# Optimization experiments

Measured on AMD Instinct MI355X. Metric: run time of the kernel, lower is better.

The kernel has to match this reference:

```python
import jax, jax.numpy as jnp
import numpy as np

N_NODES, N_EDGES, B = 50000, 400000, 64
E, NF, G, H, MLP_H, OUT, NUM_MP = 64, 128, 128, 128, 256, 1, 2


def _lin(key, fin, fout):
    W = jax.random.normal(key, (fin, fout), dtype=jnp.float32) * jnp.sqrt(2.0 / (fin + fout))
    b = jnp.full((fout,), 0.01, dtype=jnp.float32)
    return W, b


def setup_inputs() -> dict:
    key = jax.random.key(0)
    ks = jax.random.split(key, 16)
    inp = {
        "x": jax.random.normal(ks[0], (N_NODES, NF), dtype=jnp.float32),
        "edge_index": jax.random.randint(ks[1], (2, N_EDGES), 0, N_NODES, dtype=jnp.int32),
        "edge_attr": jax.random.normal(ks[2], (N_EDGES, E), dtype=jnp.float32),
        "batch": jnp.sort(jax.random.randint(ks[3], (N_NODES,), 0, B, dtype=jnp.int32)),
    }
    # EdgeModel: Lin(E+2*NF, H), Lin(H, E)
    inp["eW0"], inp["eb0"] = _lin(ks[4], E + 2 * NF, H)
    inp["eW1"], inp["eb1"] = _lin(ks[5], H, E)
    # NodeModel mlp1: Lin(E+NF, H), Lin(H, H); mlp2: Lin(H+NF, H), Lin(H, NF)
    inp["n1W0"], inp["n1b0"] = _lin(ks[6], E + NF, H)
    inp["n1W1"], inp["n1b1"] = _lin(ks[7], H, H)
    inp["n2W0"], inp["n2b0"] = _lin(ks[8], H + NF, H)
    inp["n2W1"], inp["n2b1"] = _lin(ks[9], H, NF)
    # GlobalModel mlp1: Lin(E+NF, H), Lin(H, H); mlp2: Lin(H+NF, H), Lin(H, G)
    inp["g1W0"], inp["g1b0"] = _lin(ks[10], E + NF, H)
    inp["g1W1"], inp["g1b1"] = _lin(ks[11], H, H)
    inp["g2W0"], inp["g2b0"] = _lin(ks[12], H + NF, H)
    inp["g2W1"], inp["g2b1"] = _lin(ks[13], H, G)
    # last_mlp: Lin(G, MLP_H), Lin(MLP_H, OUT)
    inp["fW0"], inp["fb0"] = _lin(ks[14], G, MLP_H)
    inp["fW1"], inp["fb1"] = _lin(ks[15], MLP_H, OUT)
    return inp


def _forward(x, edge_attr, row, col, batch,
             eW0, eb0, eW1, eb1, n1W0, n1b0, n1W1, n1b1, n2W0, n2b0, n2W1, n2b1,
             g1W0, g1b0, g1W1, g1b1, g2W0, g2b0, g2W1, g2b1, fW0, fb0, fW1, fb1):
    ea = edge_attr
    for _ in range(NUM_MP):
        # EdgeModel: gather endpoints, concat, 2-layer MLP (no activation per config)
        ea = jnp.concatenate([x[row], x[col], ea], axis=1) @ eW0 + eb0
        ea = ea @ eW1 + eb1  # [N_EDGES, E]
        # NodeModel: per-edge msg -> scatter-add to dest (col) -> node update
        m = jnp.concatenate([x[row], ea], axis=1) @ n1W0 + n1b0
        m = m @ n1W1 + n1b1
        agg = jax.ops.segment_sum(m, col, num_segments=N_NODES)  # [N_NODES, H]
        x = jnp.concatenate([x, agg], axis=1) @ n2W0 + n2b0
        x = x @ n2W1 + n2b1  # [N_NODES, NF]
        # GlobalModel: edge msg -> scatter to nodes -> pool nodes & msgs per graph
        g = jnp.concatenate([x[row], ea], axis=1) @ g1W0 + g1b0
        g = g @ g1W1 + g1b1
        gagg = jax.ops.segment_sum(g, col, num_segments=N_NODES)
        node_pool = jax.ops.segment_sum(x, batch, num_segments=B)    # [B, NF]
        msg_pool = jax.ops.segment_sum(gagg, batch, num_segments=B)  # [B, H]
        u = jnp.concatenate([node_pool, msg_pool], axis=1) @ g2W0 + g2b0
        u = u @ g2W1 + g2b1  # [B, G]
    out = (u @ fW0 + fb0) @ fW1 + fb1  # [B, OUT]
    return out


def reference(x, edge_index, edge_attr, batch,
              eW0, eb0, eW1, eb1, n1W0, n1b0, n1W1, n1b1, n2W0, n2b0, n2W1, n2b1,
              g1W0, g1b0, g1W1, g1b1, g2W0, g2b0, g2W1, g2b1, fW0, fb0, fW1, fb1):
    row, col = edge_index[0], edge_index[1]
    return _forward(x, edge_attr, row, col, batch,
                    eW0, eb0, eW1, eb1, n1W0, n1b0, n1W1, n1b1, n2W0, n2b0, n2W1, n2b1,
                    g1W0, g1b0, g1W1, g1b1, g2W0, g2b0, g2W1, g2b1, fW0, fb0, fW1, fb1)
```

## Files before the change

### kernel.cpp

```cpp
#include <hip/hip_runtime.h>
#include <hip/hip_bf16.h>

#define N_NODES 50000
#define N_EDGES 400000
#define NB 64
#define SCB 196
#define CGB 512

typedef unsigned short u16;
typedef unsigned int u32;
typedef __attribute__((ext_vector_type(8))) short s16x8;
typedef __attribute__((ext_vector_type(4))) float f32x4;

__device__ __forceinline__ u16 f2b(float f) {
  __hip_bfloat16 h = __float2bfloat16(f);
  return *reinterpret_cast<const u16*>(&h);
}
__device__ __forceinline__ float b2f(u16 u) {
  u32 v = ((u32)u) << 16;
  return *reinterpret_cast<const float*>(&v);
}
__device__ __forceinline__ s16x8 scl8(s16x8 v, float dg) {
  s16x8 r;
#pragma unroll
  for (int i = 0; i < 8; ++i) {
    float f = b2f((u16)v[i]) * dg;
    r[i] = (short)f2b(f);
  }
  return r;
}

__global__ void k_f2b(const float* __restrict__ in, u16* __restrict__ out, int n) {
  int i = blockIdx.x * 256 + threadIdx.x;
  if (i < n) out[i] = f2b(in[i]);
}

struct MMOp { const float* A; const float* B; const float* add; float* C;
              int lda, r0, ldb, K2, N, rows; };
struct MMBatch { MMOp op[13]; };

__global__ void k_mmb(MMBatch mb) {
  MMOp o = mb.op[blockIdx.y];
  int i = blockIdx.x;
  int n = threadIdx.x;
  if (i >= o.rows || n >= o.N) return;
  float acc = o.add ? o.add[(size_t)i * o.N + n] : 0.f;
  for (int k = 0; k < o.K2; ++k)
    acc = fmaf(o.A[(size_t)(o.r0 + i) * o.lda + k], o.B[(size_t)k * o.ldb + n], acc);
  o.C[(size_t)i * o.N + n] = acc;
}

__global__ void k_pack_iter(const float* __restrict__ N2a, const float* __restrict__ WadjX,
                            const float* __restrict__ A1, const float* __restrict__ WaggE,
                            const float* __restrict__ C1, const float* __restrict__ Wdegx,
                            const float* __restrict__ B1,
                            const float* __restrict__ d2, const float* __restrict__ ddeg,
                            const float* __restrict__ c0,
                            float* __restrict__ bc, float* __restrict__ bd,
                            u16* __restrict__ Wt) {
  if (blockIdx.x == 336) {
    int t = threadIdx.x;
    if (t < 192) {
      bc[t] = (t < 128) ? d2[t] : 0.f;
      bd[t] = (t < 128) ? ddeg[t] : c0[t - 128];
    }
    return;
  }
  int i = blockIdx.x * 256 + threadIdx.x;
  if (i >= 192 * 448) return;
  int n = i / 448, k = i % 448;
  float v;
  if (k < 128)      v = (n < 128) ? N2a[(size_t)k * 128 + n] : 0.f;
  else if (k < 256) { int kk = k - 128; v = (n < 128) ? WadjX[(size_t)kk * 128 + n] : A1[(size_t)kk * 64 + (n - 128)]; }
  else if (k < 320) { int kk = k - 256; v = (n < 128) ? WaggE[(size_t)kk * 128 + n] : C1[(size_t)kk * 64 + (n - 128)]; }
  else              { int kk = k - 320; v = (n < 128) ? Wdegx[(size_t)kk * 128 + n] : B1[(size_t)kk * 64 + (n - 128)]; }
  Wt[(size_t)n * 448 + k] = f2b(v);
}

__global__ void k_hist(const int* __restrict__ colv, int* __restrict__ deg) {
  int e = blockIdx.x * 256 + threadIdx.x;
  if (e < N_EDGES) atomicAdd(&deg[colv[e]], 1);
}

__global__ void k_scan1(const int* __restrict__ deg, int* __restrict__ bsum, int n) {
  __shared__ int red[256];
  int t = threadIdx.x;
  int i = blockIdx.x * 256 + t;
  red[t] = (i < n) ? deg[i] : 0;
  __syncthreads();
  for (int s = 128; s > 0; s >>= 1) {
    if (t < s) red[t] += red[t + s];
    __syncthreads();
  }
  if (t == 0) bsum[blockIdx.x] = red[0];
}

__global__ void k_scan2(int* __restrict__ bsum, int nb) {
  __shared__ int sh[256];
  int t = threadIdx.x;
  sh[t] = (t < nb) ? bsum[t] : 0;
  __syncthreads();
  for (int d = 1; d < 256; d <<= 1) {
    int v = (t >= d) ? sh[t - d] : 0;
    __syncthreads();
    sh[t] += v;
    __syncthreads();
  }
  if (t < nb) bsum[t] = sh[t];
}

__global__ void k_scan3(const int* __restrict__ deg, const int* __restrict__ bsum,
                        int* __restrict__ rowptr, int* __restrict__ cursor,
                        float* __restrict__ degf, int n) {
  __shared__ int sh[256];
  int t = threadIdx.x;
  int i = blockIdx.x * 256 + t;
  int d = (i < n) ? deg[i] : 0;
  sh[t] = d;
  __syncthreads();
  for (int s = 1; s < 256; s <<= 1) {
    int v = (t >= s) ? sh[t - s] : 0;
    __syncthreads();
    sh[t] += v;
    __syncthreads();
  }
  int base = (blockIdx.x > 0) ? bsum[blockIdx.x - 1] : 0;
  int ex = base + sh[t] - d;
  if (i < n) {
    rowptr[i] = ex;
    cursor[i] = ex;
    degf[i] = (float)d;
    if (i == n - 1) rowptr[n] = ex + d;
  }
}

__global__ void k_fill(const int* __restrict__ rowv, const int* __restrict__ colv,
                       const int* __restrict__ batch, int* __restrict__ cursor,
                       int* __restrict__ crow, int* __restrict__ ceid,
                       float* __restrict__ cnt) {
  int i = blockIdx.x * 256 + threadIdx.x;
  if (i >= N_EDGES) return;
  int c = colv[i];
  int r = rowv[i];
  int pos = atomicAdd(&cursor[c], 1);
  crow[pos] = r;
  ceid[pos] = i;
  atomicAdd(&cnt[(size_t)r * 64 + batch[c]], 1.0f);
}

__global__ __launch_bounds__(256)
void k_cntpool(const float* __restrict__ cnt, const u16* __restrict__ xb,
               float* __restrict__ Ppart,
               const u16* __restrict__ aggE, const float* __restrict__ degf,
               const int* __restrict__ batch,
               float* __restrict__ npool, float* __restrict__ PaggE,
               float* __restrict__ pdeg, int n) {
  __shared__ float cs[8][64];
  int t = threadIdx.x;
  if (blockIdx.x < CGB) {
    int c = t & 127, half = t >> 7;
    float acc[32];
#pragma unroll
    for (int q = 0; q < 32; ++q) acc[q] = 0.f;
    int span = (N_NODES + CGB - 1) / CGB;
    int v0 = blockIdx.x * span;
    int v1 = v0 + span; if (v1 > N_NODES) v1 = N_NODES;
    for (int vt = v0; vt < v1; vt += 8) {
      int nv = v1 - vt; if (nv > 8) nv = 8;
      for (int idx = t; idx < nv * 64; idx += 256)
        cs[idx >> 6][idx & 63] = cnt[(size_t)(vt + (idx >> 6)) * 64 + (idx & 63)];
      __syncthreads();
      for (int j = 0; j < nv; ++j) {
        float xv = b2f(xb[(size_t)(vt + j) * 128 + c]);
#pragma unroll
        for (int q = 0; q < 32; ++q) acc[q] = fmaf(cs[j][half * 32 + q], xv, acc[q]);
      }
      __syncthreads();
    }
#pragma unroll
    for (int q = 0; q < 32; ++q)
      Ppart[(size_t)blockIdx.x * 8192 + (size_t)(half * 32 + q) * 128 + c] = acc[q];
  } else {
    int n0 = (blockIdx.x - CGB) * 128;
    if (n0 >= n) return;
    int n1 = n0 + 128; if (n1 > n) n1 = n;
    float acc = 0.f;
    int cur = batch[n0];
    for (int i = n0; i < n1; ++i) {
      int bi = batch[i];
      if (bi != cur) {
        if (t < 128) atomicAdd(&npool[cur * 128 + t], acc);
        else if (t < 192) atomicAdd(&PaggE[cur * 64 + (t - 128)], acc);
        else if (t == 192) atomicAdd(&pdeg[cur], acc);
        acc = 0.f; cur = bi;
      }
      if (t < 128) acc += b2f(xb[(size_t)i * 128 + t]);
      else if (t < 192) acc += b2f(aggE[(size_t)i * 64 + (t - 128)]);
      else if (t == 192) acc += degf[i];
    }
    if (t < 128) atomicAdd(&npool[cur * 128 + t], acc);
    else if (t < 192) atomicAdd(&PaggE[cur * 64 + (t - 128)], acc);
    else if (t == 192) atomicAdd(&pdeg[cur], acc);
  }
}

template<bool DOE>
__global__ void k_agg(const u16* __restrict__ xb, const float* __restrict__ eaf,
                      const int* __restrict__ rowptr, const int* __restrict__ crow,
                      const int* __restrict__ ceid,
                      u16* __restrict__ outX, u16* __restrict__ outE) {
  int wpb = blockDim.x >> 6;
  int w = blockIdx.x * wpb + (threadIdx.x >> 6);
  int l = threadIdx.x & 63;
  int nw = gridDim.x * wpb;
  for (int v = w; v < N_NODES; v += nw) {
    int s = rowptr[v], e1 = rowptr[v + 1];
    float ax0 = 0.f, ax1 = 0.f, ae = 0.f;
    int i = s;
    for (; i + 7 < e1; i += 8) {
      u32 a[8]; float ev[8];
#pragma unroll
      for (int j = 0; j < 8; ++j)
        a[j] = *reinterpret_cast<const u32*>(&xb[(size_t)crow[i + j] * 128 + l * 2]);
      if (DOE) {
#pragma unroll
        for (int j = 0; j < 8; ++j)
          ev[j] = eaf[(size_t)ceid[i + j] * 64 + l];
      }
#pragma unroll
      for (int j = 0; j < 8; ++j) {
        ax0 += b2f((u16)(a[j] & 0xffff));
        ax1 += b2f((u16)(a[j] >> 16));
        if (DOE) ae += ev[j];
      }
    }
    for (; i + 3 < e1; i += 4) {
      u32 a[4]; float ev[4];
#pragma unroll
      for (int j = 0; j < 4; ++j)
        a[j] = *reinterpret_cast<const u32*>(&xb[(size_t)crow[i + j] * 128 + l * 2]);
      if (DOE) {
#pragma unroll
        for (int j = 0; j < 4; ++j)
          ev[j] = eaf[(size_t)ceid[i + j] * 64 + l];
      }
#pragma unroll
      for (int j = 0; j < 4; ++j) {
        ax0 += b2f((u16)(a[j] & 0xffff));
        ax1 += b2f((u16)(a[j] >> 16));
        if (DOE) ae += ev[j];
      }
    }
    for (; i < e1; ++i) {
      u32 a = *reinterpret_cast<const u32*>(&xb[(size_t)crow[i] * 128 + l * 2]);
      ax0 += b2f((u16)(a & 0xffff));
      ax1 += b2f((u16)(a >> 16));
      if (DOE) ae += eaf[(size_t)ceid[i] * 64 + l];
    }
    u32 pk = ((u32)f2b(ax1) << 16) | (u32)f2b(ax0);
    *reinterpret_cast<u32*>(&outX[(size_t)v * 128 + l * 2]) = pk;
    if (DOE) outE[(size_t)v * 64 + l] = f2b(ae);
  }
}

struct Chunks { const u16* src[7]; int width[7]; int koff[7]; int scl[7]; };

__global__ __launch_bounds__(256)
void gemm_fused3(const u16* __restrict__ Wt,
                 const float* __restrict__ bc, const float* __restrict__ bd,
                 const float* __restrict__ degf, Chunks ch, int M,
                 u16* __restrict__ outb0, u16* __restrict__ outb1)
{
  constexpr int LDA = 72;
  __shared__ u16 Bs[192 * LDA];
  const int t = threadIdx.x;
  const int wv = t >> 6, lane = t & 63, lr = lane & 15, lg = lane >> 4;
  const int bm0 = blockIdx.x * 64;
  const int wb = wv * 16;

  f32x4 acc[12];
#pragma unroll
  for (int f = 0; f < 12; ++f) acc[f] = (f32x4){0.f, 0.f, 0.f, 0.f};

  int arow = bm0 + wb + lr;
  if (arow >= M) arow = M - 1;
  const float dg = degf[arow];

  const int br0 = t >> 2;
  const int bo  = (t & 3) * 16;

#pragma unroll
  for (int c = 0; c < 7; ++c) {
    const u16* ap = ch.src[c] + (size_t)arow * ch.width[c] + ch.koff[c];
    s16x8 af0 = *reinterpret_cast<const s16x8*>(ap + lg * 8);
    s16x8 af1 = *reinterpret_cast<const s16x8*>(ap + 32 + lg * 8);
    if (ch.scl[c]) { af0 = scl8(af0, dg); af1 = scl8(af1, dg); }

    __syncthreads();
#pragma unroll
    for (int p = 0; p < 3; ++p) {
      const u16* bp = Wt + (size_t)(p * 64 + br0) * 448 + c * 64 + bo;
      uint4 b0 = *reinterpret_cast<const uint4*>(bp);
      uint4 b1 = *reinterpret_cast<const uint4*>(bp + 8);
      *reinterpret_cast<uint4*>(&Bs[(p * 64 + br0) * LDA + bo])     = b0;
      *reinterpret_cast<uint4*>(&Bs[(p * 64 + br0) * LDA + bo + 8]) = b1;
    }
    __syncthreads();

#pragma unroll
    for (int f = 0; f < 12; ++f) {
      s16x8 bf = *reinterpret_cast<const s16x8*>(&Bs[(f * 16 + lr) * LDA + lg * 8]);
      acc[f] = __builtin_amdgcn_mfma_f32_16x16x32_bf16(af0, bf, acc[f], 0, 0, 0);
    }
#pragma unroll
    for (int f = 0; f < 12; ++f) {
      s16x8 bf = *reinterpret_cast<const s16x8*>(&Bs[(f * 16 + lr) * LDA + 32 + lg * 8]);
      acc[f] = __builtin_amdgcn_mfma_f32_16x16x32_bf16(af1, bf, acc[f], 0, 0, 0);
    }
  }

  __syncthreads();
  u16 (*Cs)[200] = reinterpret_cast<u16(*)[200]>(Bs);
#pragma unroll
  for (int rr = 0; rr < 4; ++rr) {
    int lrow = wb + lg * 4 + rr;
    int grow = bm0 + lrow;
    float dgr = degf[(grow < M) ? grow : (M - 1)];
#pragma unroll
    for (int f = 0; f < 12; ++f) {
      int col = f * 16 + lr;
      float v = acc[f][rr] + bc[col] + dgr * bd[col];
      Cs[lrow][col] = f2b(v);
    }
  }
  __syncthreads();

#pragma unroll
  for (int p = 0; p < 4; ++p) {
    int r = p * 16 + (t >> 4), c = (t & 15) * 8;
    if (bm0 + r < M)
      *reinterpret_cast<uint4*>(&outb0[(size_t)(bm0 + r) * 128 + c]) =
          *reinterpret_cast<const uint4*>(&Cs[r][c]);
  }
#pragma unroll
  for (int p = 0; p < 2; ++p) {
    int r = p * 32 + (t >> 3), c = (t & 7) * 8;
    if (bm0 + r < M)
      *reinterpret_cast<uint4*>(&outb1[(size_t)(bm0 + r) * 64 + c]) =
          *reinterpret_cast<const uint4*>(&Cs[r][128 + c]);
  }
}

__global__ void k_head(const float* __restrict__ npool, const float* __restrict__ Ppart,
                       const float* __restrict__ PaggE, const float* __restrict__ pdeg,
                       const float* __restrict__ G1a, const float* __restrict__ G1b,
                       const float* __restrict__ e1,
                       const float* __restrict__ g2W0, const float* __restrict__ g2b0,
                       const float* __restrict__ g2W1, const float* __restrict__ g2b1,
                       const float* __restrict__ fW0, const float* __restrict__ fb0,
                       const float* __restrict__ fW1, const float* __restrict__ fb1,
                       float* __restrict__ out) {
  __shared__ float padj[128], r0[256], r1[128], r2[128], r3[256], red[256];
  int b = blockIdx.x, t = threadIdx.x;
  if (t < 128) {
    float s = 0.f;
    for (int j = 0; j < CGB; ++j) s += Ppart[(size_t)j * 8192 + (size_t)b * 128 + t];
    padj[t] = s;
  }
  __syncthreads();
  if (t < 128) {
    float a = pdeg[b] * e1[t];
    for (int k = 0; k < 128; ++k) a = fmaf(padj[k], G1a[(size_t)k * 128 + t], a);
    for (int k = 0; k < 64;  ++k) a = fmaf(PaggE[(size_t)b * 64 + k],  G1b[(size_t)k * 128 + t], a);
    r0[128 + t] = a;
    r0[t] = npool[(size_t)b * 128 + t];
  }
  __syncthreads();
  if (t < 128) {
    float a = g2b0[t];
    for (int k = 0; k < 256; ++k) a = fmaf(r0[k], g2W0[(size_t)k * 128 + t], a);
    r1[t] = a;
  }
  __syncthreads();
  if (t < 128) {
    float a = g2b1[t];
    for (int k = 0; k < 128; ++k) a = fmaf(r1[k], g2W1[(size_t)k * 128 + t], a);
    r2[t] = a;
  }
  __syncthreads();
  {
    float a = fb0[t];
    for (int k = 0; k < 128; ++k) a = fmaf(r2[k], fW0[(size_t)k * 256 + t], a);
    r3[t] = a;
  }
  __syncthreads();
  red[t] = r3[t] * fW1[t];
  __syncthreads();
  for (int s = 128; s > 0; s >>= 1) {
    if (t < s) red[t] += red[t + s];
    __syncthreads();
  }
  if (t == 0) out[b] = red[0] + fb1[0];
}

extern "C" void kernel_launch(void* const* d_in, const int* in_sizes, int n_in,
                              void* d_out, int out_size, void* d_ws, size_t ws_size,
                              hipStream_t stream) {
  const float* x     = (const float*)d_in[0];
  const int*   eidx  = (const int*)d_in[1];
  const float* eattr = (const float*)d_in[2];
  const int*   batch = (const int*)d_in[3];
  const float* eW0 = (const float*)d_in[4];  const float* eb0 = (const float*)d_in[5];
  const float* eW1 = (const float*)d_in[6];  const float* eb1 = (const float*)d_in[7];
  const float* n1W0 = (const float*)d_in[8]; const float* n1b0 = (const float*)d_in[9];
  const float* n1W1 = (const float*)d_in[10];const float* n1b1 = (const float*)d_in[11];
  const float* n2W0 = (const float*)d_in[12];const float* n2b0 = (const float*)d_in[13];
  const float* n2W1 = (const float*)d_in[14];const float* n2b1 = (const float*)d_in[15];
  const float* g1W0 = (const float*)d_in[16];const float* g1b0 = (const float*)d_in[17];
  const float* g1W1 = (const float*)d_in[18];const float* g1b1 = (const float*)d_in[19];
  const float* g2W0 = (const float*)d_in[20];const float* g2b0 = (const float*)d_in[21];
  const float* g2W1 = (const float*)d_in[22];const float* g2b1 = (const float*)d_in[23];
  const float* fW0 = (const float*)d_in[24]; const float* fb0 = (const float*)d_in[25];
  const float* fW1 = (const float*)d_in[26]; const float* fb1 = (const float*)d_in[27];

  const int* rowv = eidx;
  const int* colv = eidx + N_EDGES;

  char* ws = (char*)d_ws;
  size_t off = 0;
  auto alloc = [&](size_t bytes) -> void* {
    void* p = ws + off; off = (off + bytes + 255) & ~(size_t)255; return p;
  };
  u16*   x_b    = (u16*)alloc((size_t)N_NODES * 128 * 2);
  u16*   adjX_b = (u16*)alloc((size_t)N_NODES * 128 * 2);
  u16*   aggE_b = (u16*)alloc((size_t)N_NODES * 64 * 2);
  float* degf   = (float*)alloc((size_t)N_NODES * 4);
  int*   rowptr = (int*)alloc((size_t)(N_NODES + 1) * 4);
  int*   crow   = (int*)alloc((size_t)N_EDGES * 4);
  int*   ceid   = (int*)alloc((size_t)N_EDGES * 4);
  int*   bsum   = (int*)alloc((size_t)256 * 4);
  float* Ppart  = (float*)alloc((size_t)CGB * 8192 * 4);
  char*  zstart = ws + off;
  int*   cursor = (int*)alloc((size_t)N_NODES * 4);
  float* cnt    = (float*)alloc((size_t)N_NODES * 64 * 4);
  float* npool  = (float*)alloc((size_t)NB * 128 * 4);
  float* PaggE  = (float*)alloc((size_t)NB * 64 * 4);
  float* pdeg   = (float*)alloc((size_t)NB * 4);
  size_t zbytes = (size_t)((ws + off) - zstart);
  float* N1a   = (float*)alloc(128 * 128 * 4);
  float* N1b   = (float*)alloc(64 * 128 * 4);
  float* N2a   = (float*)alloc(128 * 128 * 4);
  float* N2b   = (float*)alloc(128 * 128 * 4);
  float* A1    = (float*)alloc(128 * 64 * 4);
  float* B1    = (float*)alloc(128 * 64 * 4);
  float* C1    = (float*)alloc(64 * 64 * 4);
  float* G1a   = (float*)alloc(128 * 128 * 4);
  float* G1b   = (float*)alloc(64 * 128 * 4);
  float* T1    = (float*)alloc(64 * 128 * 4);
  float* U1    = (float*)alloc(128 * 128 * 4);
  float* WadjX = (float*)alloc(128 * 128 * 4);
  float* WaggE = (float*)alloc(64 * 128 * 4);
  float* Wdegx = (float*)alloc(128 * 128 * 4);
  float* c0    = (float*)alloc(64 * 4);
  float* d1    = (float*)alloc(128 * 4);
  float* d2    = (float*)alloc(128 * 4);
  float* q2    = (float*)alloc(128 * 4);
  float* ddeg  = (float*)alloc(128 * 4);
  float* e1    = (float*)alloc(128 * 4);
  float* bc    = (float*)alloc(192 * 4);
  float* bd    = (float*)alloc(192 * 4);
  u16*   BigWt = (u16*)alloc((size_t)192 * 448 * 2);
  (void)ws_size; (void)in_sizes; (void)n_in; (void)out_size;

  hipMemsetAsync(zstart, 0, zbytes, stream);

  k_f2b<<<(N_NODES * 128 + 255) / 256, 256, 0, stream>>>(x, x_b, N_NODES * 128);

  {
    MMBatch L1{};
    L1.op[0]  = {n1W0, n1W1, nullptr, N1a, 128, 0,   128, 128, 128, 128};
    L1.op[1]  = {n1W0, n1W1, nullptr, N1b, 128, 128, 128, 128, 128, 64};
    L1.op[2]  = {n2W0, n2W1, nullptr, N2a, 128, 0,   128, 128, 128, 128};
    L1.op[3]  = {n2W0, n2W1, nullptr, N2b, 128, 128, 128, 128, 128, 128};
    L1.op[4]  = {eW0,  eW1,  nullptr, A1,  128, 0,   64,  128, 64,  128};
    L1.op[5]  = {eW0,  eW1,  nullptr, B1,  128, 128, 64,  128, 64,  128};
    L1.op[6]  = {eW0,  eW1,  nullptr, C1,  128, 256, 64,  128, 64,  64};
    L1.op[7]  = {g1W0, g1W1, nullptr, G1a, 128, 0,   128, 128, 128, 128};
    L1.op[8]  = {g1W0, g1W1, nullptr, G1b, 128, 128, 128, 128, 128, 64};
    L1.op[9]  = {eb0,  eW1,  eb1,     c0,  128, 0,   64,  128, 64,  1};
    L1.op[10] = {n1b0, n1W1, n1b1,    d1,  128, 0,   128, 128, 128, 1};
    L1.op[11] = {n2b0, n2W1, n2b1,    d2,  128, 0,   128, 128, 128, 1};
    L1.op[12] = {g1b0, g1W1, g1b1,    e1,  128, 0,   128, 128, 128, 1};
    k_mmb<<<dim3(128, 13), 128, 0, stream>>>(L1);

    MMBatch L2{};
    L2.op[0] = {N1b, N2b, nullptr, T1, 128, 0, 128, 128, 128, 64};
    L2.op[1] = {N1a, N2b, nullptr, U1, 128, 0, 128, 128, 128, 128};
    L2.op[2] = {c0,  N1b, d1,      q2, 64,  0, 128, 64,  128, 1};
    for (int j = 3; j < 13; ++j) L2.op[j] = {nullptr, nullptr, nullptr, nullptr, 0, 0, 0, 0, 0, 0};
    k_mmb<<<dim3(128, 3), 128, 0, stream>>>(L2);

    MMBatch L3{};
    L3.op[0] = {A1, T1, U1,      WadjX, 64,  0, 128, 64,  128, 128};
    L3.op[1] = {C1, T1, nullptr, WaggE, 64,  0, 128, 64,  128, 64};
    L3.op[2] = {B1, T1, nullptr, Wdegx, 64,  0, 128, 64,  128, 128};
    L3.op[3] = {q2, N2b, nullptr, ddeg, 128, 0, 128, 128, 128, 1};
    for (int j = 4; j < 13; ++j) L3.op[j] = {nullptr, nullptr, nullptr, nullptr, 0, 0, 0, 0, 0, 0};
    k_mmb<<<dim3(128, 4), 128, 0, stream>>>(L3);
  }
  k_pack_iter<<<337, 256, 0, stream>>>(N2a, WadjX, A1, WaggE, C1, Wdegx, B1,
                                       d2, ddeg, c0, bc, bd, BigWt);

  k_hist<<<(N_EDGES + 255) / 256, 256, 0, stream>>>(colv, cursor);
  k_scan1<<<SCB, 256, 0, stream>>>(cursor, bsum, N_NODES);
  k_scan2<<<1, 256, 0, stream>>>(bsum, SCB);
  k_scan3<<<SCB, 256, 0, stream>>>(cursor, bsum, rowptr, cursor, degf, N_NODES);
  k_fill<<<(N_EDGES + 255) / 256, 256, 0, stream>>>(rowv, colv, batch, cursor, crow, ceid, cnt);

  const int GM = (N_NODES + 63) / 64;

  Chunks chIter;
  chIter.src[0] = x_b;    chIter.width[0] = 128; chIter.koff[0] = 0;  chIter.scl[0] = 0;
  chIter.src[1] = x_b;    chIter.width[1] = 128; chIter.koff[1] = 64; chIter.scl[1] = 0;
  chIter.src[2] = adjX_b; chIter.width[2] = 128; chIter.koff[2] = 0;  chIter.scl[2] = 0;
  chIter.src[3] = adjX_b; chIter.width[3] = 128; chIter.koff[3] = 64; chIter.scl[3] = 0;
  chIter.src[4] = aggE_b; chIter.width[4] = 64;  chIter.koff[4] = 0;  chIter.scl[4] = 0;
  chIter.src[5] = x_b;    chIter.width[5] = 128; chIter.koff[5] = 0;  chIter.scl[5] = 1;
  chIter.src[6] = x_b;    chIter.width[6] = 128; chIter.koff[6] = 64; chIter.scl[6] = 1;

  k_agg<true><<<2048, 256, 0, stream>>>(x_b, eattr, rowptr, crow, ceid, adjX_b, aggE_b);
  gemm_fused3<<<GM, 256, 0, stream>>>(BigWt, bc, bd, degf, chIter, N_NODES, x_b, aggE_b);
  k_agg<false><<<2048, 256, 0, stream>>>(x_b, nullptr, rowptr, crow, ceid, adjX_b, nullptr);
  gemm_fused3<<<GM, 256, 0, stream>>>(BigWt, bc, bd, degf, chIter, N_NODES, x_b, aggE_b);

  k_cntpool<<<CGB + (N_NODES + 127) / 128, 256, 0, stream>>>(
      cnt, x_b, Ppart, aggE_b, degf, batch, npool, PaggE, pdeg, N_NODES);

  k_head<<<NB, 256, 0, stream>>>(npool, Ppart, PaggE, pdeg, G1a, G1b, e1,
                                 g2W0, g2b0, g2W1, g2b1, fW0, fb0, fW1, fb1,
                                 (float*)d_out);
}
```

Baseline: 401.6 us.

## Permute edge attributes to CSR order in bf16 and fuse histogram into x conversion

The fill kernel now runs one wavefront per edge and writes each edge's attribute row, converted to bf16, into CSR (destination-sorted) order. The aggregation kernel can then read edge features contiguously instead of gathering scattered fp32 rows through an edge-id indirection, and the ceid array is dropped. The degree histogram is merged into the x-to-bf16 conversion launch, and the count-pool block count doubles. This adds a full extra pass over edge_attr plus a 51MB write during the fill, and bf16 rounding of edge features happens before summation.

Measured after the change: 475.7 us. 18.4% more time.

```diff
diff --git a/kernel.cpp b/kernel.cpp
--- a/kernel.cpp
+++ b/kernel.cpp
@@ -5,7 +5,8 @@
 #define N_EDGES 400000
 #define NB 64
 #define SCB 196
-#define CGB 512
+#define CGB 1024
+#define XFB 25000
 
 typedef unsigned short u16;
 typedef unsigned int u32;
@@ -30,9 +31,15 @@
   return r;
 }
 
-__global__ void k_f2b(const float* __restrict__ in, u16* __restrict__ out, int n) {
-  int i = blockIdx.x * 256 + threadIdx.x;
-  if (i < n) out[i] = f2b(in[i]);
+__global__ void k_prep(const float* __restrict__ x, u16* __restrict__ xb,
+                       const int* __restrict__ colv, int* __restrict__ deg) {
+  if (blockIdx.x < XFB) {
+    int i = blockIdx.x * 256 + threadIdx.x;
+    xb[i] = f2b(x[i]);
+  } else {
+    int e = (blockIdx.x - XFB) * 256 + threadIdx.x;
+    if (e < N_EDGES) atomicAdd(&deg[colv[e]], 1);
+  }
 }
 
 struct MMOp { const float* A; const float* B; const float* add; float* C;
@@ -77,11 +84,6 @@
   Wt[(size_t)n * 448 + k] = f2b(v);
 }
 
-__global__ void k_hist(const int* __restrict__ colv, int* __restrict__ deg) {
-  int e = blockIdx.x * 256 + threadIdx.x;
-  if (e < N_EDGES) atomicAdd(&deg[colv[e]], 1);
-}
-
 __global__ void k_scan1(const int* __restrict__ deg, int* __restrict__ bsum, int n) {
   __shared__ int red[256];
   int t = threadIdx.x;
@@ -135,17 +137,22 @@
 }
 
 __global__ void k_fill(const int* __restrict__ rowv, const int* __restrict__ colv,
-                       const int* __restrict__ batch, int* __restrict__ cursor,
-                       int* __restrict__ crow, int* __restrict__ ceid,
-                       float* __restrict__ cnt) {
-  int i = blockIdx.x * 256 + threadIdx.x;
-  if (i >= N_EDGES) return;
-  int c = colv[i];
-  int r = rowv[i];
-  int pos = atomicAdd(&cursor[c], 1);
-  crow[pos] = r;
-  ceid[pos] = i;
-  atomicAdd(&cnt[(size_t)r * 64 + batch[c]], 1.0f);
+                       const int* __restrict__ batch, const float* __restrict__ eattr,
+                       int* __restrict__ cursor, int* __restrict__ crow,
+                       u16* __restrict__ eaperm, float* __restrict__ cnt) {
+  int e = blockIdx.x * 4 + (threadIdx.x >> 6);
+  if (e >= N_EDGES) return;
+  int l = threadIdx.x & 63;
+  int c = colv[e];
+  int pos;
+  if (l == 0) {
+    int r = rowv[e];
+    pos = atomicAdd(&cursor[c], 1);
+    crow[pos] = r;
+    atomicAdd(&cnt[(size_t)r * 64 + batch[c]], 1.0f);
+  }
+  pos = __shfl(pos, 0);
+  eaperm[(size_t)pos * 64 + l] = f2b(eattr[(size_t)e * 64 + l]);
 }
 
 __global__ __launch_bounds__(256)
@@ -205,9 +212,8 @@
 }
 
 template<bool DOE>
-__global__ void k_agg(const u16* __restrict__ xb, const float* __restrict__ eaf,
+__global__ void k_agg(const u16* __restrict__ xb, const u16* __restrict__ eaperm,
                       const int* __restrict__ rowptr, const int* __restrict__ crow,
-                      const int* __restrict__ ceid,
                       u16* __restrict__ outX, u16* __restrict__ outE) {
   int wpb = blockDim.x >> 6;
   int w = blockIdx.x * wpb + (threadIdx.x >> 6);
@@ -225,7 +231,7 @@
       if (DOE) {
 #pragma unroll
         for (int j = 0; j < 8; ++j)
-          ev[j] = eaf[(size_t)ceid[i + j] * 64 + l];
+          ev[j] = b2f(eaperm[(size_t)(i + j) * 64 + l]);
       }
 #pragma unroll
       for (int j = 0; j < 8; ++j) {
@@ -242,7 +248,7 @@
       if (DOE) {
 #pragma unroll
         for (int j = 0; j < 4; ++j)
-          ev[j] = eaf[(size_t)ceid[i + j] * 64 + l];
+          ev[j] = b2f(eaperm[(size_t)(i + j) * 64 + l]);
       }
 #pragma unroll
       for (int j = 0; j < 4; ++j) {
@@ -255,7 +261,7 @@
       u32 a = *reinterpret_cast<const u32*>(&xb[(size_t)crow[i] * 128 + l * 2]);
       ax0 += b2f((u16)(a & 0xffff));
       ax1 += b2f((u16)(a >> 16));
-      if (DOE) ae += eaf[(size_t)ceid[i] * 64 + l];
+      if (DOE) ae += b2f(eaperm[(size_t)i * 64 + l]);
     }
     u32 pk = ((u32)f2b(ax1) << 16) | (u32)f2b(ax0);
     *reinterpret_cast<u32*>(&outX[(size_t)v * 128 + l * 2]) = pk;
@@ -434,10 +440,10 @@
   u16*   x_b    = (u16*)alloc((size_t)N_NODES * 128 * 2);
   u16*   adjX_b = (u16*)alloc((size_t)N_NODES * 128 * 2);
   u16*   aggE_b = (u16*)alloc((size_t)N_NODES * 64 * 2);
+  u16*   eaperm = (u16*)alloc((size_t)N_EDGES * 64 * 2);
   float* degf   = (float*)alloc((size_t)N_NODES * 4);
   int*   rowptr = (int*)alloc((size_t)(N_NODES + 1) * 4);
   int*   crow   = (int*)alloc((size_t)N_EDGES * 4);
-  int*   ceid   = (int*)alloc((size_t)N_EDGES * 4);
   int*   bsum   = (int*)alloc((size_t)256 * 4);
   float* Ppart  = (float*)alloc((size_t)CGB * 8192 * 4);
   char*  zstart = ws + off;
@@ -474,7 +480,7 @@
 
   hipMemsetAsync(zstart, 0, zbytes, stream);
 
-  k_f2b<<<(N_NODES * 128 + 255) / 256, 256, 0, stream>>>(x, x_b, N_NODES * 128);
+  k_prep<<<XFB + (N_EDGES + 255) / 256, 256, 0, stream>>>(x, x_b, colv, cursor);
 
   {
     MMBatch L1{};
@@ -511,11 +517,10 @@
   k_pack_iter<<<337, 256, 0, stream>>>(N2a, WadjX, A1, WaggE, C1, Wdegx, B1,
                                        d2, ddeg, c0, bc, bd, BigWt);
 
-  k_hist<<<(N_EDGES + 255) / 256, 256, 0, stream>>>(colv, cursor);
   k_scan1<<<SCB, 256, 0, stream>>>(cursor, bsum, N_NODES);
   k_scan2<<<1, 256, 0, stream>>>(bsum, SCB);
   k_scan3<<<SCB, 256, 0, stream>>>(cursor, bsum, rowptr, cursor, degf, N_NODES);
-  k_fill<<<(N_EDGES + 255) / 256, 256, 0, stream>>>(rowv, colv, batch, cursor, crow, ceid, cnt);
+  k_fill<<<N_EDGES / 4, 256, 0, stream>>>(rowv, colv, batch, eattr, cursor, crow, eaperm, cnt);
 
   const int GM = (N_NODES + 63) / 64;
 
@@ -528,9 +533,9 @@
   chIter.src[5] = x_b;    chIter.width[5] = 128; chIter.koff[5] = 0;  chIter.scl[5] = 1;
   chIter.src[6] = x_b;    chIter.width[6] = 128; chIter.koff[6] = 64; chIter.scl[6] = 1;
 
-  k_agg<true><<<2048, 256, 0, stream>>>(x_b, eattr, rowptr, crow, ceid, adjX_b, aggE_b);
+  k_agg<true><<<2048, 256, 0, stream>>>(x_b, eaperm, rowptr, crow, adjX_b, aggE_b);
   gemm_fused3<<<GM, 256, 0, stream>>>(BigWt, bc, bd, degf, chIter, N_NODES, x_b, aggE_b);
-  k_agg<false><<<2048, 256, 0, stream>>>(x_b, nullptr, rowptr, crow, ceid, adjX_b, nullptr);
+  k_agg<false><<<2048, 256, 0, stream>>>(x_b, nullptr, rowptr, crow, adjX_b, nullptr);
   gemm_fused3<<<GM, 256, 0, stream>>>(BigWt, bc, bd, degf, chIter, N_NODES, x_b, aggE_b);
 
   k_cntpool<<<CGB + (N_NODES + 127) / 128, 256, 0, stream>>>(
```

## Pre-convert edge attributes to bf16 and fuse prep kernels with degree histogram

Applied to the files above, without the earlier changes.

Adds a combined prep kernel that converts x and edge_attr to bf16 and computes the in-degree histogram in one launch, replacing the separate f2b and hist kernels. The first aggregation pass now gathers bf16 edge attributes instead of fp32, halving bytes per random gather. It also doubles the pooling grid constant. The trade-off is an extra full streaming pass over edge_attr (read fp32, write bf16) plus extra workspace, with some precision loss on the aggregated edge features.

Result: slower. 462.7 us (+15.2%).

```diff
diff --git a/kernel.cpp b/kernel.cpp
--- a/kernel.cpp
+++ b/kernel.cpp
@@ -5,7 +5,9 @@
 #define N_EDGES 400000
 #define NB 64
 #define SCB 196
-#define CGB 512
+#define CGB 1024
+#define XFB 25000
+#define EFB 100000
 
 typedef unsigned short u16;
 typedef unsigned int u32;
@@ -30,9 +32,20 @@
   return r;
 }
 
-__global__ void k_f2b(const float* __restrict__ in, u16* __restrict__ out, int n) {
-  int i = blockIdx.x * 256 + threadIdx.x;
-  if (i < n) out[i] = f2b(in[i]);
+__global__ void k_prep(const float* __restrict__ x, u16* __restrict__ xb,
+                       const float* __restrict__ eattr, u16* __restrict__ ea_b,
+                       const int* __restrict__ colv, int* __restrict__ deg) {
+  int b = blockIdx.x;
+  if (b < XFB) {
+    int i = b * 256 + threadIdx.x;
+    xb[i] = f2b(x[i]);
+  } else if (b < XFB + EFB) {
+    int i = (b - XFB) * 256 + threadIdx.x;
+    ea_b[i] = f2b(eattr[i]);
+  } else {
+    int e = (b - XFB - EFB) * 256 + threadIdx.x;
+    if (e < N_EDGES) atomicAdd(&deg[colv[e]], 1);
+  }
 }
 
 struct MMOp { const float* A; const float* B; const float* add; float* C;
@@ -75,11 +88,6 @@
   else if (k < 320) { int kk = k - 256; v = (n < 128) ? WaggE[(size_t)kk * 128 + n] : C1[(size_t)kk * 64 + (n - 128)]; }
   else              { int kk = k - 320; v = (n < 128) ? Wdegx[(size_t)kk * 128 + n] : B1[(size_t)kk * 64 + (n - 128)]; }
   Wt[(size_t)n * 448 + k] = f2b(v);
-}
-
-__global__ void k_hist(const int* __restrict__ colv, int* __restrict__ deg) {
-  int e = blockIdx.x * 256 + threadIdx.x;
-  if (e < N_EDGES) atomicAdd(&deg[colv[e]], 1);
 }
 
 __global__ void k_scan1(const int* __restrict__ deg, int* __restrict__ bsum, int n) {
@@ -205,7 +213,7 @@
 }
 
 template<bool DOE>
-__global__ void k_agg(const u16* __restrict__ xb, const float* __restrict__ eaf,
+__global__ void k_agg(const u16* __restrict__ xb, const u16* __restrict__ ea_b,
                       const int* __restrict__ rowptr, const int* __restrict__ crow,
                       const int* __restrict__ ceid,
                       u16* __restrict__ outX, u16* __restrict__ outE) {
@@ -225,7 +233,7 @@
       if (DOE) {
 #pragma unroll
         for (int j = 0; j < 8; ++j)
-          ev[j] = eaf[(size_t)ceid[i + j] * 64 + l];
+          ev[j] = b2f(ea_b[(size_t)ceid[i + j] * 64 + l]);
       }
 #pragma unroll
       for (int j = 0; j < 8; ++j) {
@@ -242,7 +250,7 @@
       if (DOE) {
 #pragma unroll
         for (int j = 0; j < 4; ++j)
-          ev[j] = eaf[(size_t)ceid[i + j] * 64 + l];
+          ev[j] = b2f(ea_b[(size_t)ceid[i + j] * 64 + l]);
       }
 #pragma unroll
       for (int j = 0; j < 4; ++j) {
@@ -255,7 +263,7 @@
       u32 a = *reinterpret_cast<const u32*>(&xb[(size_t)crow[i] * 128 + l * 2]);
       ax0 += b2f((u16)(a & 0xffff));
       ax1 += b2f((u16)(a >> 16));
-      if (DOE) ae += eaf[(size_t)ceid[i] * 64 + l];
+      if (DOE) ae += b2f(ea_b[(size_t)ceid[i] * 64 + l]);
     }
     u32 pk = ((u32)f2b(ax1) << 16) | (u32)f2b(ax0);
     *reinterpret_cast<u32*>(&outX[(size_t)v * 128 + l * 2]) = pk;
@@ -434,6 +442,7 @@
   u16*   x_b    = (u16*)alloc((size_t)N_NODES * 128 * 2);
   u16*   adjX_b = (u16*)alloc((size_t)N_NODES * 128 * 2);
   u16*   aggE_b = (u16*)alloc((size_t)N_NODES * 64 * 2);
+  u16*   ea_b   = (u16*)alloc((size_t)N_EDGES * 64 * 2);
   float* degf   = (float*)alloc((size_t)N_NODES * 4);
   int*   rowptr = (int*)alloc((size_t)(N_NODES + 1) * 4);
   int*   crow   = (int*)alloc((size_t)N_EDGES * 4);
@@ -474,7 +483,7 @@
 
   hipMemsetAsync(zstart, 0, zbytes, stream);
 
-  k_f2b<<<(N_NODES * 128 + 255) / 256, 256, 0, stream>>>(x, x_b, N_NODES * 128);
+  k_prep<<<XFB + EFB + (N_EDGES + 255) / 256, 256, 0, stream>>>(x, x_b, eattr, ea_b, colv, cursor);
 
   {
     MMBatch L1{};
@@ -511,7 +520,6 @@
   k_pack_iter<<<337, 256, 0, stream>>>(N2a, WadjX, A1, WaggE, C1, Wdegx, B1,
                                        d2, ddeg, c0, bc, bd, BigWt);
 
-  k_hist<<<(N_EDGES + 255) / 256, 256, 0, stream>>>(colv, cursor);
   k_scan1<<<SCB, 256, 0, stream>>>(cursor, bsum, N_NODES);
   k_scan2<<<1, 256, 0, stream>>>(bsum, SCB);
   k_scan3<<<SCB, 256, 0, stream>>>(cursor, bsum, rowptr, cursor, degf, N_NODES);
@@ -528,7 +536,7 @@
   chIter.src[5] = x_b;    chIter.width[5] = 128; chIter.koff[5] = 0;  chIter.scl[5] = 1;
   chIter.src[6] = x_b;    chIter.width[6] = 128; chIter.koff[6] = 64; chIter.scl[6] = 1;
 
-  k_agg<true><<<2048, 256, 0, stream>>>(x_b, eattr, rowptr, crow, ceid, adjX_b, aggE_b);
+  k_agg<true><<<2048, 256, 0, stream>>>(x_b, ea_b, rowptr, crow, ceid, adjX_b, aggE_b);
   gemm_fused3<<<GM, 256, 0, stream>>>(BigWt, bc, bd, degf, chIter, N_NODES, x_b, aggE_b);
   k_agg<false><<<2048, 256, 0, stream>>>(x_b, nullptr, rowptr, crow, ceid, adjX_b, nullptr);
   gemm_fused3<<<GM, 256, 0, stream>>>(BigWt, bc, bd, degf, chIter, N_NODES, x_b, aggE_b);
```
